# Performance work log

Hardware: AMD Instinct MI355X
Metric: run time of the kernel (lower is better)

Reference implementation:

```python
import jax, jax.numpy as jnp
import numpy as np

LATENT_DIM = 256
CODEBOOK_SIZE = 8192
COMMITMENT_WEIGHT = 0.25
CODEBOOK_WEIGHT = 1.0


def setup_inputs() -> dict:
    key = jax.random.key(0)
    k1, k2 = jax.random.split(key)
    latents = jax.random.normal(k1, (16, 1024, LATENT_DIM), dtype=jnp.float32)
    patch_mask = jnp.ones((16, 1024), dtype=jnp.float32)
    # nn.init.uniform_(codebook.weight, -1/K, 1/K)
    codebook = jax.random.uniform(
        k2, (CODEBOOK_SIZE, LATENT_DIM), dtype=jnp.float32,
        minval=-1.0 / CODEBOOK_SIZE, maxval=1.0 / CODEBOOK_SIZE)
    return {"latents": latents, "patch_mask": patch_mask, "codebook": codebook}


def reference(latents, patch_mask, codebook):
    B, P, D = latents.shape
    flat = latents.reshape(-1, D)  # [N, D]
    # squared euclidean distances [N, K]
    distances = (
        jnp.sum(flat * flat, axis=1, keepdims=True)
        + jnp.sum(codebook * codebook, axis=1)
        - 2.0 * flat @ codebook.T
    )
    symbol_ids = jnp.argmin(distances, axis=1)          # [N]
    quantized = codebook[symbol_ids].reshape(B, P, D)   # [B, P, D]
    symbol_ids = symbol_ids.reshape(B, P)

    st_quantized = latents + jax.lax.stop_gradient(quantized - latents)
    commitment_loss = jnp.mean((latents - jax.lax.stop_gradient(quantized)) ** 2) * COMMITMENT_WEIGHT
    codebook_loss = jnp.mean((quantized - jax.lax.stop_gradient(latents)) ** 2) * CODEBOOK_WEIGHT

    # perplexity: masked codeword usage histogram without materializing one-hot
    denom = jnp.maximum(jnp.sum(patch_mask), 1.0)
    avg_probs = jax.ops.segment_sum(
        patch_mask.reshape(-1), symbol_ids.reshape(-1),
        num_segments=CODEBOOK_SIZE) / denom
    perplexity = jnp.exp(-jnp.sum(avg_probs * jnp.log(avg_probs + 1e-8)))

    return symbol_ids, quantized, st_quantized, commitment_loss, codebook_loss, perplexity
```

## Files before the change

kernel.cpp:

```cpp
#include <hip/hip_runtime.h>
#include <math.h>

#define DD 256
#define KK 8192
#define NN 16384
#define MT 32
#define RPW 8
#define NCH 16
#define NT 512
#define NBLOCKS 512
#define RSTRIDE 260

#define OUT_IDS   0
#define OUT_Q     16384
#define OUT_ST    4210688
#define OUT_COMMIT 8404992
#define OUT_CBL    8404993
#define OUT_PERP   8404994

__device__ __forceinline__ float rlane(float v, int l) {
    return __int_as_float(__builtin_amdgcn_readlane(__float_as_int(v), l));
}

__device__ __forceinline__ float np_block128_sumsq(const float* p) {
    #pragma clang fp contract(off)
    float r0 = p[0] * p[0], r1 = p[1] * p[1], r2 = p[2] * p[2], r3 = p[3] * p[3];
    float r4 = p[4] * p[4], r5 = p[5] * p[5], r6 = p[6] * p[6], r7 = p[7] * p[7];
    for (int i = 8; i < 128; i += 8) {
        r0 = r0 + p[i + 0] * p[i + 0];
        r1 = r1 + p[i + 1] * p[i + 1];
        r2 = r2 + p[i + 2] * p[i + 2];
        r3 = r3 + p[i + 3] * p[i + 3];
        r4 = r4 + p[i + 4] * p[i + 4];
        r5 = r5 + p[i + 5] * p[i + 5];
        r6 = r6 + p[i + 6] * p[i + 6];
        r7 = r7 + p[i + 7] * p[i + 7];
    }
    return ((r0 + r1) + (r2 + r3)) + ((r4 + r5) + (r6 + r7));
}

__device__ __forceinline__ float np_pairwise256_sumsq(const float* a) {
    #pragma clang fp contract(off)
    float s0 = np_block128_sumsq(a);
    float s1 = np_block128_sumsq(a + 128);
    return s0 + s1;
}

__global__ __launch_bounds__(256) void rowsumsq(const float* __restrict__ A,
                                                float* __restrict__ out) {
    __shared__ __align__(16) float sA[64][RSTRIDE];
    const int tid = threadIdx.x;
    const int base = blockIdx.x * 64;
    #pragma unroll
    for (int i = 0; i < 16; ++i) {
        int g = i * 256 + tid;
        int row = g >> 6, d4 = g & 63;
        float4 v = reinterpret_cast<const float4*>(A)[(size_t)(base + row) * (DD / 4) + d4];
        *reinterpret_cast<float4*>(&sA[row][d4 * 4]) = v;
    }
    __syncthreads();
    if (tid < 64) out[base + tid] = np_pairwise256_sumsq(sA[tid]);
}

__global__ __launch_bounds__(256) void cb_transpose(const float* __restrict__ CB,
                                                    float4* __restrict__ CBt) {
    const int id = blockIdx.x * 256 + threadIdx.x;
    const int p   = id >> 13;
    const int col = id & (KK - 1);
    CBt[id] = *reinterpret_cast<const float4*>(CB + (size_t)col * DD + p * 4);
}

__global__ __launch_bounds__(256) void vq_main(const float* __restrict__ X,
                                               const float4* __restrict__ CBt,
                                               const float* __restrict__ c2,
                                               const float* __restrict__ x2,
                                               const float* __restrict__ mask,
                                               float* __restrict__ out,
                                               float* __restrict__ hist) {
    __shared__ int row_id[MT];

    const int tid  = threadIdx.x;
    const int lane = tid & 63;
    const int wid  = tid >> 6;
    const int block_row = blockIdx.x * MT;

    const float* xbase = X + (size_t)(block_row + wid * RPW + (lane & 7)) * DD
                           + (lane >> 3) * 4;

    float x2r[RPW];
    #pragma unroll
    for (int rr = 0; rr < RPW; ++rr) x2r[rr] = x2[block_row + wid * RPW + rr];

    float best[RPW];
    int   besti[RPW];
    #pragma unroll
    for (int rr = 0; rr < RPW; ++rr) { best[rr] = 3.4e38f; besti[rr] = 0; }

    const float4* cbt_lane = CBt + lane;

    for (int ch = 0; ch < NCH; ++ch) {
        float c2v[8];
        #pragma unroll
        for (int j = 0; j < 8; ++j) c2v[j] = c2[ch * NT + lane + 64 * j];

        float acc[8][8];
        #pragma unroll
        for (int rr = 0; rr < 8; ++rr)
            #pragma unroll
            for (int j = 0; j < 8; ++j) acc[rr][j] = 0.0f;

        const float4* cbase = cbt_lane + ch * NT;

        for (int b = 0; b < 8; ++b) {
            const float4 xp = *reinterpret_cast<const float4*>(xbase + b * 32);
            #pragma unroll
            for (int t = 0; t < 8; ++t) {
                const int p = b * 8 + t;
                const float4* src = cbase + (size_t)p * KK;
                float4 cc[8];
                #pragma unroll
                for (int j = 0; j < 8; ++j) cc[j] = src[64 * j];
                #pragma unroll
                for (int rr = 0; rr < 8; ++rr) {
                    const int rl = t * 8 + rr;
                    const float sx = rlane(xp.x, rl);
                    const float sy = rlane(xp.y, rl);
                    const float sz = rlane(xp.z, rl);
                    const float sw = rlane(xp.w, rl);
                    #pragma unroll
                    for (int j = 0; j < 8; ++j) {
                        acc[rr][j] = fmaf(sx, cc[j].x, acc[rr][j]);
                        acc[rr][j] = fmaf(sy, cc[j].y, acc[rr][j]);
                        acc[rr][j] = fmaf(sz, cc[j].z, acc[rr][j]);
                        acc[rr][j] = fmaf(sw, cc[j].w, acc[rr][j]);
                    }
                }
            }
        }

        #pragma unroll
        for (int rr = 0; rr < 8; ++rr) {
            #pragma unroll
            for (int j = 0; j < 8; ++j) {
                const int col = ch * NT + lane + 64 * j;
                float t1 = x2r[rr] + c2v[j];
                float sc = t1 - 2.0f * acc[rr][j];
                if (sc < best[rr] || (sc == best[rr] && col < besti[rr])) {
                    best[rr] = sc; besti[rr] = col;
                }
            }
        }
    }

    #pragma unroll
    for (int rr = 0; rr < RPW; ++rr) {
        float b = best[rr];
        int  bi = besti[rr];
        #pragma unroll
        for (int m = 32; m > 0; m >>= 1) {
            float b2 = __shfl_xor(b, m, 64);
            int   i2 = __shfl_xor(bi, m, 64);
            if (b2 < b || (b2 == b && i2 < bi)) { b = b2; bi = i2; }
        }
        if (lane == 0) row_id[wid * RPW + rr] = bi;
    }
    __syncthreads();

    if (tid < MT) {
        int bi = row_id[tid];
        out[OUT_IDS + block_row + tid] = (float)bi;
        atomicAdd(&hist[bi], mask[block_row + tid]);
    }
}

__global__ __launch_bounds__(256) void vq_gather(const float* __restrict__ X,
                                                 const float* __restrict__ CB,
                                                 float* __restrict__ out,
                                                 float* __restrict__ partial) {
    __shared__ int   row_id[32];
    __shared__ float wsum[4];
    const int tid  = threadIdx.x;
    const int lane = tid & 63;
    const int wid  = tid >> 6;
    const int block_row = blockIdx.x * 32;

    if (tid < 32) row_id[tid] = (int)out[OUT_IDS + block_row + tid];
    __syncthreads();

    float msep = 0.0f;
    float* outq  = out + OUT_Q;
    float* outst = out + OUT_ST;
    #pragma unroll
    for (int i = 0; i < 8; ++i) {
        int g2 = i * 256 + tid;
        int row = g2 >> 6;
        int d4  = g2 & 63;
        int id  = row_id[row];
        float4 q = reinterpret_cast<const float4*>(CB)[(size_t)id * (DD / 4) + d4];
        float4 x = reinterpret_cast<const float4*>(X)[(size_t)(block_row + row) * (DD / 4) + d4];
        float4 st;
        st.x = x.x + (q.x - x.x);
        st.y = x.y + (q.y - x.y);
        st.z = x.z + (q.z - x.z);
        st.w = x.w + (q.w - x.w);
        float dx = x.x - q.x; msep = fmaf(dx, dx, msep);
        dx = x.y - q.y; msep = fmaf(dx, dx, msep);
        dx = x.z - q.z; msep = fmaf(dx, dx, msep);
        dx = x.w - q.w; msep = fmaf(dx, dx, msep);
        size_t o = (size_t)(block_row + row) * (DD / 4) + d4;
        reinterpret_cast<float4*>(outq)[o]  = q;
        reinterpret_cast<float4*>(outst)[o] = st;
    }
    #pragma unroll
    for (int off = 32; off > 0; off >>= 1) msep += __shfl_down(msep, off, 64);
    if (lane == 0) wsum[wid] = msep;
    __syncthreads();
    if (tid == 0) partial[blockIdx.x] = wsum[0] + wsum[1] + wsum[2] + wsum[3];
}

__global__ __launch_bounds__(256) void vq_finalize(const float* __restrict__ partial,
                                                   const float* __restrict__ hist,
                                                   float* __restrict__ out) {
    __shared__ double red[256];
    const int tid = threadIdx.x;

    double ps = 0.0;
    for (int j = tid; j < NBLOCKS; j += 256) ps += (double)partial[j];
    red[tid] = ps;
    __syncthreads();
    for (int s = 128; s > 0; s >>= 1) {
        if (tid < s) red[tid] += red[tid + s];
        __syncthreads();
    }
    double mse_sum = red[0];
    __syncthreads();

    double hs = 0.0;
    for (int j = tid; j < KK; j += 256) hs += (double)hist[j];
    red[tid] = hs;
    __syncthreads();
    for (int s = 128; s > 0; s >>= 1) {
        if (tid < s) red[tid] += red[tid + s];
        __syncthreads();
    }
    double denom = red[0] > 1.0 ? red[0] : 1.0;
    __syncthreads();

    double ent = 0.0;
    for (int j = tid; j < KK; j += 256) {
        double p = (double)hist[j] / denom;
        ent += p * log(p + 1e-8);
    }
    red[tid] = ent;
    __syncthreads();
    for (int s = 128; s > 0; s >>= 1) {
        if (tid < s) red[tid] += red[tid + s];
        __syncthreads();
    }

    if (tid == 0) {
        double mse = mse_sum / (double)((size_t)NN * DD);
        out[OUT_COMMIT] = (float)(mse * 0.25);
        out[OUT_CBL]    = (float)mse;
        out[OUT_PERP]   = (float)exp(-red[0]);
    }
}

extern "C" void kernel_launch(void* const* d_in, const int* in_sizes, int n_in,
                              void* d_out, int out_size, void* d_ws, size_t ws_size,
                              hipStream_t stream) {
    const float* latents = (const float*)d_in[0];
    const float* mask    = (const float*)d_in[1];
    const float* cb      = (const float*)d_in[2];
    float* out = (float*)d_out;

    float* hist    = (float*)d_ws;
    float* partial = hist + KK;
    float* c2      = partial + NBLOCKS;
    float* x2      = c2 + KK;

    float4* cbt = reinterpret_cast<float4*>(out + OUT_Q);

    hipMemsetAsync(d_ws, 0, KK * sizeof(float), stream);
    rowsumsq<<<KK / 64, 256, 0, stream>>>(cb, c2);
    rowsumsq<<<NN / 64, 256, 0, stream>>>(latents, x2);
    cb_transpose<<<(64 * KK) / 256, 256, 0, stream>>>(cb, cbt);
    vq_main<<<NBLOCKS, 256, 0, stream>>>(latents, cbt, c2, x2, mask, out, hist);
    vq_gather<<<NBLOCKS, 256, 0, stream>>>(latents, cb, out, partial);
    vq_finalize<<<1, 256, 0, stream>>>(partial, hist, out);
}
```

Before: 941.4 us.

## Split codebook across wave pairs and read latents via scalar loads

Each block now handles 16 rows instead of 32, and its four waves form two groups that each scan half the codebook chunks. Partial argmin results are merged through shared memory. Latent values are read with wave-uniform addresses, which lets the compiler use scalar loads instead of readlane broadcasts. This doubles the grid size and raises parallelism, but each codebook tile is now reused by fewer rows, so total codebook traffic from memory and cache rises.

```diff
diff --git a/kernel.cpp b/kernel.cpp
--- a/kernel.cpp
+++ b/kernel.cpp
@@ -4,10 +4,11 @@
 #define DD 256
 #define KK 8192
 #define NN 16384
-#define MT 32
+#define MT 16
 #define RPW 8
-#define NCH 16
 #define NT 512
+#define NCHG 8
+#define NBM (NN / MT)
 #define NBLOCKS 512
 #define RSTRIDE 260
 
@@ -17,10 +18,6 @@
 #define OUT_COMMIT 8404992
 #define OUT_CBL    8404993
 #define OUT_PERP   8404994
-
-__device__ __forceinline__ float rlane(float v, int l) {
-    return __int_as_float(__builtin_amdgcn_readlane(__float_as_int(v), l));
-}
 
 __device__ __forceinline__ float np_block128_sumsq(const float* p) {
     #pragma clang fp contract(off)
@@ -77,19 +74,24 @@
                                                const float* __restrict__ mask,
                                                float* __restrict__ out,
                                                float* __restrict__ hist) {
-    __shared__ int row_id[MT];
+    __shared__ float gbest[2][MT];
+    __shared__ int   gidx[2][MT];
 
     const int tid  = threadIdx.x;
     const int lane = tid & 63;
     const int wid  = tid >> 6;
+    const int widu = __builtin_amdgcn_readfirstlane(wid);
+    const int g    = wid >> 1;
+    const int gu   = widu >> 1;
+    const int wg   = wid & 1;
+    const int wgu  = widu & 1;
     const int block_row = blockIdx.x * MT;
 
-    const float* xbase = X + (size_t)(block_row + wid * RPW + (lane & 7)) * DD
-                           + (lane >> 3) * 4;
+    const float* xr = X + (size_t)(block_row + wgu * RPW) * DD;
 
     float x2r[RPW];
     #pragma unroll
-    for (int rr = 0; rr < RPW; ++rr) x2r[rr] = x2[block_row + wid * RPW + rr];
+    for (int rr = 0; rr < RPW; ++rr) x2r[rr] = x2[block_row + wg * RPW + rr];
 
     float best[RPW];
     int   besti[RPW];
@@ -98,10 +100,11 @@
 
     const float4* cbt_lane = CBt + lane;
 
-    for (int ch = 0; ch < NCH; ++ch) {
+    for (int ch = 0; ch < NCHG; ++ch) {
+        const int chg = gu * NCHG + ch;
         float c2v[8];
         #pragma unroll
-        for (int j = 0; j < 8; ++j) c2v[j] = c2[ch * NT + lane + 64 * j];
+        for (int j = 0; j < 8; ++j) c2v[j] = c2[chg * NT + lane + 64 * j];
 
         float acc[8][8];
         #pragma unroll
@@ -109,30 +112,32 @@
             #pragma unroll
             for (int j = 0; j < 8; ++j) acc[rr][j] = 0.0f;
 
-        const float4* cbase = cbt_lane + ch * NT;
+        const float4* cbase = cbt_lane + (size_t)chg * NT;
 
         for (int b = 0; b < 8; ++b) {
-            const float4 xp = *reinterpret_cast<const float4*>(xbase + b * 32);
             #pragma unroll
             for (int t = 0; t < 8; ++t) {
                 const int p = b * 8 + t;
                 const float4* src = cbase + (size_t)p * KK;
-                float4 cc[8];
                 #pragma unroll
-                for (int j = 0; j < 8; ++j) cc[j] = src[64 * j];
-                #pragma unroll
-                for (int rr = 0; rr < 8; ++rr) {
-                    const int rl = t * 8 + rr;
-                    const float sx = rlane(xp.x, rl);
-                    const float sy = rlane(xp.y, rl);
-                    const float sz = rlane(xp.z, rl);
-                    const float sw = rlane(xp.w, rl);
+                for (int jh = 0; jh < 2; ++jh) {
+                    float4 cc[4];
                     #pragma unroll
-                    for (int j = 0; j < 8; ++j) {
-                        acc[rr][j] = fmaf(sx, cc[j].x, acc[rr][j]);
-                        acc[rr][j] = fmaf(sy, cc[j].y, acc[rr][j]);
-                        acc[rr][j] = fmaf(sz, cc[j].z, acc[rr][j]);
-                        acc[rr][j] = fmaf(sw, cc[j].w, acc[rr][j]);
+                    for (int j = 0; j < 4; ++j) cc[j] = src[64 * (jh * 4 + j)];
+                    #pragma unroll
+                    for (int rr = 0; rr < 8; ++rr) {
+                        const float sx = xr[rr * DD + p * 4 + 0];
+                        const float sy = xr[rr * DD + p * 4 + 1];
+                        const float sz = xr[rr * DD + p * 4 + 2];
+                        const float sw = xr[rr * DD + p * 4 + 3];
+                        #pragma unroll
+                        for (int j = 0; j < 4; ++j) {
+                            float& a = acc[rr][jh * 4 + j];
+                            a = fmaf(sx, cc[j].x, a);
+                            a = fmaf(sy, cc[j].y, a);
+                            a = fmaf(sz, cc[j].z, a);
+                            a = fmaf(sw, cc[j].w, a);
+                        }
                     }
                 }
             }
@@ -142,7 +147,7 @@
         for (int rr = 0; rr < 8; ++rr) {
             #pragma unroll
             for (int j = 0; j < 8; ++j) {
-                const int col = ch * NT + lane + 64 * j;
+                const int col = chg * NT + lane + 64 * j;
                 float t1 = x2r[rr] + c2v[j];
                 float sc = t1 - 2.0f * acc[rr][j];
                 if (sc < best[rr] || (sc == best[rr] && col < besti[rr])) {
@@ -162,12 +167,16 @@
             int   i2 = __shfl_xor(bi, m, 64);
             if (b2 < b || (b2 == b && i2 < bi)) { b = b2; bi = i2; }
         }
-        if (lane == 0) row_id[wid * RPW + rr] = bi;
+        if (lane == 0) {
+            gbest[g][wg * RPW + rr] = b;
+            gidx [g][wg * RPW + rr] = bi;
+        }
     }
     __syncthreads();
 
     if (tid < MT) {
-        int bi = row_id[tid];
+        const float b0 = gbest[0][tid], b1 = gbest[1][tid];
+        const int bi = (b1 < b0) ? gidx[1][tid] : gidx[0][tid];
         out[OUT_IDS + block_row + tid] = (float)bi;
         atomicAdd(&hist[bi], mask[block_row + tid]);
     }
@@ -285,7 +294,7 @@
     rowsumsq<<<KK / 64, 256, 0, stream>>>(cb, c2);
     rowsumsq<<<NN / 64, 256, 0, stream>>>(latents, x2);
     cb_transpose<<<(64 * KK) / 256, 256, 0, stream>>>(cb, cbt);
-    vq_main<<<NBLOCKS, 256, 0, stream>>>(latents, cbt, c2, x2, mask, out, hist);
+    vq_main<<<NBM, 256, 0, stream>>>(latents, cbt, c2, x2, mask, out, hist);
     vq_gather<<<NBLOCKS, 256, 0, stream>>>(latents, cb, out, partial);
     vq_finalize<<<1, 256, 0, stream>>>(partial, hist, out);
 }
```

New measurement: 934.1 us. Within noise of the previous version (-0.8%).
